# Performance work log

Measured on AMD Instinct MI355X. Metric: run time of the kernel, lower is better.

Reference implementation:

```python
import jax, jax.numpy as jnp
import numpy as np

HIDDEN = 1024
HEADS = 16
HEAD = HIDDEN // HEADS
EXPAND = 4096
EPS = 1e-5


def layer_norm(x, g, b):
    mu = jnp.mean(x, axis=-1, keepdims=True)
    var = jnp.mean((x - mu) ** 2, axis=-1, keepdims=True)
    return (x - mu) * jax.lax.rsqrt(var + EPS) * g + b


def setup_inputs() -> dict:
    key = jax.random.key(0)
    ks = jax.random.split(key, 12)
    s = 0.02
    return {
        "x": jax.random.normal(ks[0], (4, 2048, HIDDEN), dtype=jnp.float32),
        "Wqkv": jax.random.normal(ks[1], (HIDDEN, 3 * HIDDEN), dtype=jnp.float32) * s,
        "bqkv": jnp.zeros((3 * HIDDEN,), jnp.float32),
        "Wproj": jax.random.normal(ks[2], (HIDDEN, HIDDEN), dtype=jnp.float32) * s,
        "bproj": jnp.zeros((HIDDEN,), jnp.float32),
        "W1": jax.random.normal(ks[3], (HIDDEN, EXPAND), dtype=jnp.float32) * s,
        "b1": jnp.zeros((EXPAND,), jnp.float32),
        "W2": jax.random.normal(ks[4], (EXPAND, HIDDEN), dtype=jnp.float32) * s,
        "b2": jnp.zeros((HIDDEN,), jnp.float32),
        "g1": jnp.ones((HIDDEN,), jnp.float32),
        "be1": jnp.zeros((HIDDEN,), jnp.float32),
        "g2": jnp.ones((HIDDEN,), jnp.float32),
        "be2": jnp.zeros((HIDDEN,), jnp.float32),
    }


def attention(x, Wqkv, bqkv, Wproj, bproj):
    B, L, _ = x.shape
    qkv = (x @ Wqkv + bqkv).reshape(B, L, 3, HEADS, HEAD)
    q, k, v = [qkv[:, :, i].transpose(0, 2, 1, 3) for i in range(3)]  # [B,H,L,D]
    attn = jnp.einsum("bnld,bnkd->bnlk", q, k) / np.sqrt(HEAD).astype(np.float32)
    attn = jax.nn.softmax(attn, axis=-1)
    o = jnp.einsum("bnlk,bnkd->bnld", attn, v)
    o = o.transpose(0, 2, 1, 3).reshape(B, L, HIDDEN)
    return o @ Wproj + bproj


def reference(x, Wqkv, bqkv, Wproj, bproj, W1, b1, W2, b2, g1, be1, g2, be2):
    # post-norm transformer block (pre_norm=False), dropout=0 (eval)
    h = layer_norm(x + attention(x, Wqkv, bqkv, Wproj, bproj), g1, be1)
    ff = jax.nn.gelu(h @ W1 + b1, approximate=False) @ W2 + b2
    return layer_norm(h + ff, g2, be2)
```

## Files before the change

kernel.cpp:

```cpp
#include <hip/hip_runtime.h>
#include <hip/hip_bf16.h>
#include <math.h>


typedef __bf16 bf16_t;
typedef __bf16 bf16x8 __attribute__((ext_vector_type(8)));
typedef __bf16 bf16x4 __attribute__((ext_vector_type(4)));
typedef float f32x4 __attribute__((ext_vector_type(4)));
typedef float f32x16 __attribute__((ext_vector_type(16)));

#define HID   1024
#define NHEAD 16
#define HD    64
#define EXPD  4096
#define LSEQ  2048
#define BATCH 4
#define MROWS (BATCH * LSEQ)

#if __has_builtin(__builtin_amdgcn_exp2f)
#define EXP2F __builtin_amdgcn_exp2f
#else
#define EXP2F exp2f
#endif

__device__ __forceinline__ void gld_lds16(const bf16_t* g, bf16_t* l) {
  __builtin_amdgcn_global_load_lds(
      (const __attribute__((address_space(1))) void*)g,
      (__attribute__((address_space(3))) void*)l, 16, 0, 0);
}

template <int N>
__device__ __forceinline__ void wait_vm() {
  if constexpr (N == 8)      asm volatile("s_waitcnt vmcnt(8)" ::: "memory");
  else if constexpr (N == 6) asm volatile("s_waitcnt vmcnt(6)" ::: "memory");
  else if constexpr (N == 4) asm volatile("s_waitcnt vmcnt(4)" ::: "memory");
  else if constexpr (N == 3) asm volatile("s_waitcnt vmcnt(3)" ::: "memory");
  else                       asm volatile("s_waitcnt vmcnt(0)" ::: "memory");
}

__device__ __forceinline__ void swap32(unsigned& a, unsigned& b) {
#if __has_builtin(__builtin_amdgcn_permlane32_swap)
  auto r = __builtin_amdgcn_permlane32_swap(a, b, false, false);
  a = r[0]; b = r[1];
#else
  bool hiL = ((threadIdx.x & 63) >= 32);
  unsigned pa = (unsigned)__shfl_xor((int)a, 32, 64);
  unsigned pb = (unsigned)__shfl_xor((int)b, 32, 64);
  unsigned na = hiL ? pb : a;
  unsigned nb = hiL ? b : pa;
  a = na; b = nb;
#endif
}

__device__ __forceinline__ unsigned pk_bf16(float lo, float hi) {
  bf16_t l = (bf16_t)lo, h = (bf16_t)hi;
  unsigned short ul, uh;
  __builtin_memcpy(&ul, &l, 2);
  __builtin_memcpy(&uh, &h, 2);
  return (unsigned)ul | ((unsigned)uh << 16);
}

__global__ __launch_bounds__(256) void cvt_bf16(const float* __restrict__ in,
                                                bf16_t* __restrict__ out, int n4) {
  int i = blockIdx.x * 256 + threadIdx.x;
  if (i >= n4) return;
  float4 v = ((const float4*)in)[i];
  bf16x4 o;
  o[0] = (bf16_t)v.x; o[1] = (bf16_t)v.y; o[2] = (bf16_t)v.z; o[3] = (bf16_t)v.w;
  ((bf16x4*)out)[i] = o;
}

__global__ __launch_bounds__(256) void transpose_cvt(const float* __restrict__ W,
                                                     bf16_t* __restrict__ Wt,
                                                     int K, int N) {
  __shared__ float tile[32][33];
  int n0 = blockIdx.x * 32, k0 = blockIdx.y * 32;
  int tx = threadIdx.x & 31, ty = threadIdx.x >> 5;
#pragma unroll
  for (int i = 0; i < 32; i += 8)
    tile[ty + i][tx] = W[(size_t)(k0 + ty + i) * N + n0 + tx];
  __syncthreads();
#pragma unroll
  for (int i = 0; i < 32; i += 8)
    Wt[(size_t)(n0 + ty + i) * K + k0 + tx] = (bf16_t)tile[tx][ty + i];
}

__global__ __launch_bounds__(256) void transpose_v(const bf16_t* __restrict__ qkvb,
                                                   bf16_t* __restrict__ vT) {
  __shared__ bf16_t tile[64][65];
  const int l0 = blockIdx.x * 64;
  const int bh = blockIdx.y;
  const int b = bh >> 4, h = bh & 15;
  const int tx = threadIdx.x & 63, ty = threadIdx.x >> 6;
  const bf16_t* src = qkvb + ((size_t)(b * LSEQ + l0)) * 3072 + 2048 + h * 64;
#pragma unroll
  for (int i = 0; i < 16; ++i) {
    int l = ty + 4 * i;
    tile[l][tx] = src[(size_t)l * 3072 + tx];
  }
  __syncthreads();
  bf16_t* dst = vT + ((size_t)bh * HD) * LSEQ + l0;
#pragma unroll
  for (int i = 0; i < 16; ++i) {
    int d = ty + 4 * i;
    dst[(size_t)d * LSEQ + tx] = tile[tx][d];
  }
}

template <int BM>
__global__ __launch_bounds__(512, 2) void gemm_p(const bf16_t* __restrict__ A,
                                                 const bf16_t* __restrict__ Bt,
                                                 const float* __restrict__ bias,
                                                 void* __restrict__ C,
                                                 int M, int N, int K, int mode) {
  constexpr int MI = BM / 32;
  constexpr int LOADS = (BM == 256) ? 4 : 3;
  __shared__ bf16_t As[4 * BM * 32];
  __shared__ bf16_t Bs[4 * 256 * 32];

  const int nbx = gridDim.x;
  int p = blockIdx.y * nbx + blockIdx.x;
  const int GM = 8;
  int group = p / (GM * nbx);
  int idx = p - group * (GM * nbx);
  const int by = group * GM + (idx & (GM - 1));
  const int bx = idx >> 3;
  const int n0 = bx * 256, m0 = by * BM;

  const int t = threadIdx.x;
  const int lane = t & 63, w = t >> 6;
  const int wr = w >> 2, wc = w & 3;
  const int quad = lane >> 4, l16 = lane & 15;

  f32x4 acc[MI][4];
#pragma unroll
  for (int i = 0; i < MI; ++i)
#pragma unroll
    for (int j = 0; j < 4; ++j) acc[i][j] = (f32x4){0.f, 0.f, 0.f, 0.f};

  const int r0 = t >> 2;
  const unsigned ksw = (((unsigned)t & 3u) ^ ((unsigned)(r0 >> 1) & 3u)) * 8u;
  const unsigned offR0 = (unsigned)r0 * (unsigned)K + ksw;
  const unsigned off128 = offR0 + 128u * (unsigned)K;

  const bf16_t* aB = A + (size_t)m0 * K;
  const bf16_t* bB = Bt + (size_t)n0 * K;

  unsigned aoff[MI], boff[4];
#pragma unroll
  for (int i = 0; i < MI; ++i) {
    int row = wr * (BM / 2) + 16 * i + l16;
    aoff[i] = (unsigned)(row * 32 + (quad ^ ((row >> 1) & 3)) * 8);
  }
#pragma unroll
  for (int j = 0; j < 4; ++j) {
    int row = wc * 64 + 16 * j + l16;
    boff[j] = (unsigned)(row * 32 + (quad ^ ((row >> 1) & 3)) * 8);
  }

  auto stage = [&](int slot, int kk) {
    bf16_t* Asl = As + slot * (BM * 32);
    bf16_t* Bsl = Bs + slot * (256 * 32);
    const bf16_t* aS = aB + kk;
    const bf16_t* bS = bB + kk;
    gld_lds16(aS + offR0, Asl + t * 8);
    if constexpr (BM == 256) gld_lds16(aS + off128, Asl + (t + 512) * 8);
    gld_lds16(bS + offR0, Bsl + t * 8);
    gld_lds16(bS + off128, Bsl + (t + 512) * 8);
  };

  auto compute = [&](int slot) {
    const bf16_t* Asl = As + slot * (BM * 32);
    const bf16_t* Bsl = Bs + slot * (256 * 32);
    bf16x8 af[MI], bfr[4];
#pragma unroll
    for (int i = 0; i < MI; ++i) af[i] = *(const bf16x8*)(Asl + aoff[i]);
#pragma unroll
    for (int j = 0; j < 4; ++j) bfr[j] = *(const bf16x8*)(Bsl + boff[j]);
    __builtin_amdgcn_s_setprio(1);
#pragma unroll
    for (int i = 0; i < MI; ++i)
#pragma unroll
      for (int j = 0; j < 4; ++j)
        acc[i][j] = __builtin_amdgcn_mfma_f32_16x16x32_bf16(af[i], bfr[j], acc[i][j], 0, 0, 0);
    __builtin_amdgcn_s_setprio(0);
  };

  const int NT = K >> 5;

  stage(0, 0);
  stage(1, 32);
  stage(2, 64);
  int kk = 96;

  int kt = 0;
  for (; kt < NT - 3; ++kt) {
    wait_vm<2 * LOADS>();
    __builtin_amdgcn_s_barrier();
    asm volatile("" ::: "memory");
    stage((kt + 3) & 3, kk);
    kk += 32;
    compute(kt & 3);
  }
  wait_vm<2 * LOADS>();
  __builtin_amdgcn_s_barrier();
  asm volatile("" ::: "memory");
  compute(kt & 3);
  ++kt;
  wait_vm<LOADS>();
  __builtin_amdgcn_s_barrier();
  asm volatile("" ::: "memory");
  compute(kt & 3);
  ++kt;
  wait_vm<0>();
  __builtin_amdgcn_s_barrier();
  asm volatile("" ::: "memory");
  compute(kt & 3);

#pragma unroll
  for (int i = 0; i < MI; ++i) {
    int rowb = m0 + wr * (BM / 2) + 16 * i + quad * 4;
#pragma unroll
    for (int j = 0; j < 4; ++j) {
      int col = n0 + wc * 64 + 16 * j + l16;
      float bv = bias[col];
#pragma unroll
      for (int r = 0; r < 4; ++r) {
        float v = acc[i][j][r] + bv;
        size_t idx = (size_t)(rowb + r) * N + col;
        if (mode == 0) {
          ((bf16_t*)C)[idx] = (bf16_t)v;
        } else if (mode == 1) {
          float u = v * (0.7978845608028654f + 0.0356774081f * v * v);
          float e = EXP2F(u * 2.885390082f);
          float th = (e - 1.f) / (e + 1.f);
          float gel = 0.5f * v * (1.f + th);
          ((bf16_t*)C)[idx] = (bf16_t)gel;
        } else {
          ((float*)C)[idx] = v;
        }
      }
    }
  }
}

__global__ __launch_bounds__(256) void attn_kernel(const bf16_t* __restrict__ qkv,
                                                   const bf16_t* __restrict__ vT,
                                                   bf16_t* __restrict__ ob) {
  __shared__ bf16_t smem[3 * 128 * 64];
  bf16_t* Ks  = smem;
  bf16_t* Vts = smem + 8192;
  bf16_t* Qs  = smem + 16384;
  const int qt = blockIdx.x, h = blockIdx.y, b = blockIdx.z;
  const int t = threadIdx.x, lane = t & 63, w = t >> 6;
  const int l32 = lane & 31, hi = lane >> 5;
  const size_t RS = 3 * HID;
  const int bh = b * NHEAD + h;

  const bf16_t* qbase = qkv + ((size_t)(b * LSEQ + qt * 128)) * RS + h * HD;
  const bf16_t* kbase = qkv + ((size_t)b * LSEQ) * RS + HID + h * HD;
  const bf16_t* vtbase = vT + (size_t)bh * HD * LSEQ;

#pragma unroll
  for (int s = 0; s < 4; ++s) {
    int l = t + s * 256;
    int r = l >> 3, c8 = l & 7;
    gld_lds16(qbase + (size_t)r * RS + ((c8 ^ (r & 7)) * 8), Qs + l * 8);
  }
  __syncthreads();

  const float sc = 0.18033688011112042f;
  bf16x8 bq[4];
  {
    int qrow = 32 * w + l32;
#pragma unroll
    for (int c = 0; c < 4; ++c) {
      int y = 2 * c + hi;
      bf16x8 q8 = *(const bf16x8*)(Qs + qrow * 64 + ((y ^ (qrow & 7)) * 8));
#pragma unroll
      for (int e = 0; e < 8; ++e) q8[e] = (bf16_t)((float)q8[e] * sc);
      bq[c] = q8;
    }
  }

  f32x16 accO[2];
#pragma unroll
  for (int dt = 0; dt < 2; ++dt)
#pragma unroll
    for (int e = 0; e < 16; ++e) accO[dt][e] = 0.f;
  float l_acc = 0.f;

  for (int kt = 0; kt < LSEQ / 128; ++kt) {
    __syncthreads();
#pragma unroll
    for (int s = 0; s < 4; ++s) {
      int l = t + s * 256;
      int r = l >> 3, c8 = l & 7;
      gld_lds16(kbase + (size_t)(kt * 128 + r) * RS + ((c8 ^ (r & 7)) * 8), Ks + l * 8);
      int rv = l >> 4, c16 = l & 15;
      gld_lds16(vtbase + (size_t)rv * LSEQ + kt * 128 + ((c16 ^ (rv & 7)) * 8), Vts + l * 8);
    }
    __syncthreads();

#pragma unroll
    for (int kt2 = 0; kt2 < 2; ++kt2) {
      f32x16 s0, s1;
#pragma unroll
      for (int e = 0; e < 16; ++e) { s0[e] = 0.f; s1[e] = 0.f; }
#pragma unroll
      for (int c = 0; c < 4; ++c) {
        int y = 2 * c + hi;
        int r0 = (2 * kt2 + 0) * 32 + l32;
        bf16x8 a0 = *(const bf16x8*)(Ks + r0 * 64 + ((y ^ (r0 & 7)) * 8));
        s0 = __builtin_amdgcn_mfma_f32_32x32x16_bf16(a0, bq[c], s0, 0, 0, 0);
        int r1 = (2 * kt2 + 1) * 32 + l32;
        bf16x8 a1 = *(const bf16x8*)(Ks + r1 * 64 + ((y ^ (r1 & 7)) * 8));
        s1 = __builtin_amdgcn_mfma_f32_32x32x16_bf16(a1, bq[c], s1, 0, 0, 0);
      }

      unsigned pf[2][2][4];
#pragma unroll
      for (int tile = 0; tile < 2; ++tile) {
        f32x16& sv = tile ? s1 : s0;
        float p[16];
#pragma unroll
        for (int e = 0; e < 16; ++e) { p[e] = EXP2F(sv[e]); l_acc += p[e]; }
        unsigned lo[4], hi_[4];
#pragma unroll
        for (int g = 0; g < 4; ++g) {
          lo[g] = pk_bf16(p[4 * g + 0], p[4 * g + 1]);
          hi_[g] = pk_bf16(p[4 * g + 2], p[4 * g + 3]);
        }
#pragma unroll
        for (int c2 = 0; c2 < 2; ++c2) {
          unsigned aL = lo[2 * c2], bL = lo[2 * c2 + 1];
          swap32(aL, bL);
          pf[tile][c2][0] = aL; pf[tile][c2][2] = bL;
          unsigned aH = hi_[2 * c2], bH = hi_[2 * c2 + 1];
          swap32(aH, bH);
          pf[tile][c2][1] = aH; pf[tile][c2][3] = bH;
        }
      }

#pragma unroll
      for (int dt = 0; dt < 2; ++dt)
#pragma unroll
        for (int tile = 0; tile < 2; ++tile)
#pragma unroll
          for (int c2 = 0; c2 < 2; ++c2) {
            int ktile = 2 * kt2 + tile;
            int c8v = ktile * 4 + c2 * 2 + hi;
            int rv = dt * 32 + l32;
            bf16x8 av = *(const bf16x8*)(Vts + rv * 128 + ((c8v ^ (rv & 7)) * 8));
            union { unsigned u[4]; bf16x8 v; } bp;
            bp.u[0] = pf[tile][c2][0]; bp.u[1] = pf[tile][c2][1];
            bp.u[2] = pf[tile][c2][2]; bp.u[3] = pf[tile][c2][3];
            accO[dt] = __builtin_amdgcn_mfma_f32_32x32x16_bf16(av, bp.v, accO[dt], 0, 0, 0);
          }
    }
  }

  l_acc += __shfl_xor(l_acc, 32, 64);
  float inv = 1.f / l_acc;

  __syncthreads();
  bf16_t* Osh = smem;
  {
    int q = 32 * w + l32;
#pragma unroll
    for (int dt = 0; dt < 2; ++dt)
#pragma unroll
      for (int e = 0; e < 16; ++e) {
        int d = dt * 32 + (e & 3) + 8 * (e >> 2) + 4 * hi;
        Osh[q * 68 + d] = (bf16_t)(accO[dt][e] * inv);
      }
  }
  __syncthreads();
#pragma unroll
  for (int s = 0; s < 4; ++s) {
    int l = t + s * 256;
    int r = l >> 3, c8 = l & 7;
    bf16x8 v = *(const bf16x8*)(Osh + r * 68 + c8 * 8);
    *(bf16x8*)(ob + ((size_t)(b * LSEQ + qt * 128 + r)) * HID + h * HD + c8 * 8) = v;
  }
}

__global__ __launch_bounds__(256) void resid_ln(const float* __restrict__ X,
                                                const float* __restrict__ Y,
                                                const float* __restrict__ g,
                                                const float* __restrict__ be,
                                                float* __restrict__ outf,
                                                bf16_t* __restrict__ outb) {
  const int row = blockIdx.x;
  const int t = threadIdx.x;
  float4 a = ((const float4*)X)[(size_t)row * 256 + t];
  float4 bvec = ((const float4*)Y)[(size_t)row * 256 + t];
  float v0 = a.x + bvec.x, v1 = a.y + bvec.y, v2 = a.z + bvec.z, v3 = a.w + bvec.w;
  float s = v0 + v1 + v2 + v3;
  float s2 = v0 * v0 + v1 * v1 + v2 * v2 + v3 * v3;
#pragma unroll
  for (int msk = 1; msk < 64; msk <<= 1) {
    s += __shfl_xor(s, msk, 64);
    s2 += __shfl_xor(s2, msk, 64);
  }
  __shared__ float red[8];
  int w = t >> 6;
  if ((t & 63) == 0) { red[w] = s; red[w + 4] = s2; }
  __syncthreads();
  s = red[0] + red[1] + red[2] + red[3];
  s2 = red[4] + red[5] + red[6] + red[7];
  float mu = s * (1.f / 1024.f);
  float var = s2 * (1.f / 1024.f) - mu * mu;
  float rstd = rsqrtf(var + 1e-5f);
  float4 gg = ((const float4*)g)[t];
  float4 bb = ((const float4*)be)[t];
  float o0 = (v0 - mu) * rstd * gg.x + bb.x;
  float o1 = (v1 - mu) * rstd * gg.y + bb.y;
  float o2 = (v2 - mu) * rstd * gg.z + bb.z;
  float o3 = (v3 - mu) * rstd * gg.w + bb.w;
  float4 o = {o0, o1, o2, o3};
  ((float4*)outf)[(size_t)row * 256 + t] = o;
  if (outb) {
    bf16x4 ob4;
    ob4[0] = (bf16_t)o0; ob4[1] = (bf16_t)o1; ob4[2] = (bf16_t)o2; ob4[3] = (bf16_t)o3;
    ((bf16x4*)outb)[(size_t)row * 256 + t] = ob4;
  }
}

extern "C" void kernel_launch(void* const* d_in, const int* in_sizes, int n_in,
                              void* d_out, int out_size, void* d_ws, size_t ws_size,
                              hipStream_t stream) {
  const float* x     = (const float*)d_in[0];
  const float* Wqkv  = (const float*)d_in[1];
  const float* bqkv  = (const float*)d_in[2];
  const float* Wproj = (const float*)d_in[3];
  const float* bproj = (const float*)d_in[4];
  const float* W1    = (const float*)d_in[5];
  const float* b1    = (const float*)d_in[6];
  const float* W2    = (const float*)d_in[7];
  const float* b2    = (const float*)d_in[8];
  const float* g1    = (const float*)d_in[9];
  const float* be1   = (const float*)d_in[10];
  const float* g2    = (const float*)d_in[11];
  const float* be2   = (const float*)d_in[12];
  float* out = (float*)d_out;

  char* ws = (char*)d_ws;
  size_t off = 0;
  auto alloc = [&](size_t bytes) -> char* {
    char* p = ws + off;
    off += (bytes + 255) & ~(size_t)255;
    return p;
  };
  bf16_t* wqkvT  = (bf16_t*)alloc((size_t)3072 * 1024 * 2);
  bf16_t* wprojT = (bf16_t*)alloc((size_t)1024 * 1024 * 2);
  bf16_t* w1T    = (bf16_t*)alloc((size_t)4096 * 1024 * 2);
  bf16_t* w2T    = (bf16_t*)alloc((size_t)1024 * 4096 * 2);
  char*   xb_ob  = alloc((size_t)MROWS * HID * 2);
  char*   qkv_ff = alloc((size_t)MROWS * EXPD * 2);
  char*   a_f2   = alloc((size_t)MROWS * HID * 4);
  float*  h      = (float*)alloc((size_t)MROWS * HID * 4);
  bf16_t* hb     = (bf16_t*)alloc((size_t)MROWS * HID * 2);

  bf16_t* xb    = (bf16_t*)xb_ob;
  bf16_t* ob    = (bf16_t*)xb_ob;
  bf16_t* qkvb  = (bf16_t*)qkv_ff;
  bf16_t* ff1b  = (bf16_t*)qkv_ff;
  float*  attnf = (float*)a_f2;
  float*  ff2f  = (float*)a_f2;
  bf16_t* vTg   = hb;

  dim3 blk(256);
  dim3 blk512(512);
  transpose_cvt<<<dim3(3072 / 32, 1024 / 32), blk, 0, stream>>>(Wqkv, wqkvT, 1024, 3072);
  transpose_cvt<<<dim3(1024 / 32, 1024 / 32), blk, 0, stream>>>(Wproj, wprojT, 1024, 1024);
  transpose_cvt<<<dim3(4096 / 32, 1024 / 32), blk, 0, stream>>>(W1, w1T, 1024, 4096);
  transpose_cvt<<<dim3(1024 / 32, 4096 / 32), blk, 0, stream>>>(W2, w2T, 4096, 1024);
  cvt_bf16<<<MROWS * HID / 4 / 256, blk, 0, stream>>>(x, xb, MROWS * HID / 4);

  gemm_p<256><<<dim3(3072 / 256, MROWS / 256), blk512, 0, stream>>>(xb, wqkvT, bqkv, qkvb,
                                                                    MROWS, 3072, 1024, 0);
  transpose_v<<<dim3(LSEQ / 64, BATCH * NHEAD), blk, 0, stream>>>(qkvb, vTg);
  attn_kernel<<<dim3(LSEQ / 128, NHEAD, BATCH), blk, 0, stream>>>(qkvb, vTg, ob);
  gemm_p<128><<<dim3(1024 / 256, MROWS / 128), blk512, 0, stream>>>(ob, wprojT, bproj, attnf,
                                                                    MROWS, 1024, 1024, 2);
  resid_ln<<<MROWS, blk, 0, stream>>>(x, attnf, g1, be1, h, hb);
  gemm_p<256><<<dim3(4096 / 256, MROWS / 256), blk512, 0, stream>>>(hb, w1T, b1, ff1b,
                                                                    MROWS, 4096, 1024, 1);
  gemm_p<128><<<dim3(1024 / 256, MROWS / 128), blk512, 0, stream>>>(ff1b, w2T, b2, ff2f,
                                                                    MROWS, 1024, 4096, 2);
  resid_ln<<<MROWS, blk, 0, stream>>>(h, ff2f, g2, be2, out, (bf16_t*)nullptr);
}
```

Baseline: 630.5 us.

## Restructure GEMM k-step into two barrier-separated phases interleaving loads and MFMA

Replaces the GEMM main loop with a ping-pong style k-step: each iteration splits the MFMA work into two halves of the A rows. A and B global-to-LDS prefetches are interleaved between the halves, with explicit barriers, lgkmcnt waits and sched_barriers. The kernel is also re-parameterized on BN with BM fixed at 256, so the N=1024 GEMMs use 256x128 tiles instead of 128x256. The aim is better overlap of memory traffic with matrix math, at the cost of extra barriers per k-step and more fragile synchronization.

```diff
diff --git a/kernel.cpp b/kernel.cpp
--- a/kernel.cpp
+++ b/kernel.cpp
@@ -29,13 +29,12 @@
       (__attribute__((address_space(3))) void*)l, 16, 0, 0);
 }
 
-template <int N>
-__device__ __forceinline__ void wait_vm() {
-  if constexpr (N == 8)      asm volatile("s_waitcnt vmcnt(8)" ::: "memory");
-  else if constexpr (N == 6) asm volatile("s_waitcnt vmcnt(6)" ::: "memory");
-  else if constexpr (N == 4) asm volatile("s_waitcnt vmcnt(4)" ::: "memory");
-  else if constexpr (N == 3) asm volatile("s_waitcnt vmcnt(3)" ::: "memory");
-  else                       asm volatile("s_waitcnt vmcnt(0)" ::: "memory");
+__device__ __forceinline__ void vmwait(int n) {
+  if (n == 8)      asm volatile("s_waitcnt vmcnt(8)" ::: "memory");
+  else if (n == 6) asm volatile("s_waitcnt vmcnt(6)" ::: "memory");
+  else if (n == 4) asm volatile("s_waitcnt vmcnt(4)" ::: "memory");
+  else if (n == 3) asm volatile("s_waitcnt vmcnt(3)" ::: "memory");
+  else if (n == 0) asm volatile("s_waitcnt vmcnt(0)" ::: "memory");
 }
 
 __device__ __forceinline__ void swap32(unsigned& a, unsigned& b) {
@@ -107,16 +106,19 @@
   }
 }
 
-template <int BM>
-__global__ __launch_bounds__(512, 2) void gemm_p(const bf16_t* __restrict__ A,
-                                                 const bf16_t* __restrict__ Bt,
-                                                 const float* __restrict__ bias,
-                                                 void* __restrict__ C,
-                                                 int M, int N, int K, int mode) {
+template <int BN>
+__global__ __launch_bounds__(512, 2) void gemm_8p(const bf16_t* __restrict__ A,
+                                                  const bf16_t* __restrict__ Bt,
+                                                  const float* __restrict__ bias,
+                                                  void* __restrict__ C,
+                                                  int M, int N, int K, int mode) {
+  constexpr int BM = 256;
   constexpr int MI = BM / 32;
-  constexpr int LOADS = (BM == 256) ? 4 : 3;
+  constexpr int NJ = BN / 64;
+  constexpr int BL = BN / 128;
+  constexpr int LOADS = 2 + BL;
   __shared__ bf16_t As[4 * BM * 32];
-  __shared__ bf16_t Bs[4 * 256 * 32];
+  __shared__ bf16_t Bs[4 * BN * 32];
 
   const int nbx = gridDim.x;
   int p = blockIdx.y * nbx + blockIdx.x;
@@ -125,18 +127,18 @@
   int idx = p - group * (GM * nbx);
   const int by = group * GM + (idx & (GM - 1));
   const int bx = idx >> 3;
-  const int n0 = bx * 256, m0 = by * BM;
+  const int n0 = bx * BN, m0 = by * BM;
 
   const int t = threadIdx.x;
   const int lane = t & 63, w = t >> 6;
   const int wr = w >> 2, wc = w & 3;
   const int quad = lane >> 4, l16 = lane & 15;
 
-  f32x4 acc[MI][4];
+  f32x4 acc[MI][NJ];
 #pragma unroll
   for (int i = 0; i < MI; ++i)
 #pragma unroll
-    for (int j = 0; j < 4; ++j) acc[i][j] = (f32x4){0.f, 0.f, 0.f, 0.f};
+    for (int j = 0; j < NJ; ++j) acc[i][j] = (f32x4){0.f, 0.f, 0.f, 0.f};
 
   const int r0 = t >> 2;
   const unsigned ksw = (((unsigned)t & 3u) ^ ((unsigned)(r0 >> 1) & 3u)) * 8u;
@@ -146,83 +148,95 @@
   const bf16_t* aB = A + (size_t)m0 * K;
   const bf16_t* bB = Bt + (size_t)n0 * K;
 
-  unsigned aoff[MI], boff[4];
+  unsigned aoff[MI], boff[NJ];
 #pragma unroll
   for (int i = 0; i < MI; ++i) {
     int row = wr * (BM / 2) + 16 * i + l16;
     aoff[i] = (unsigned)(row * 32 + (quad ^ ((row >> 1) & 3)) * 8);
   }
 #pragma unroll
-  for (int j = 0; j < 4; ++j) {
-    int row = wc * 64 + 16 * j + l16;
+  for (int j = 0; j < NJ; ++j) {
+    int row = wc * (BN / 4) + 16 * j + l16;
     boff[j] = (unsigned)(row * 32 + (quad ^ ((row >> 1) & 3)) * 8);
   }
 
-  auto stage = [&](int slot, int kk) {
+  auto stageA = [&](int slot, int kk) {
     bf16_t* Asl = As + slot * (BM * 32);
-    bf16_t* Bsl = Bs + slot * (256 * 32);
     const bf16_t* aS = aB + kk;
+    gld_lds16(aS + offR0, Asl + t * 8);
+    gld_lds16(aS + off128, Asl + (t + 512) * 8);
+  };
+  auto stageB = [&](int slot, int kk) {
+    bf16_t* Bsl = Bs + slot * (BN * 32);
     const bf16_t* bS = bB + kk;
-    gld_lds16(aS + offR0, Asl + t * 8);
-    if constexpr (BM == 256) gld_lds16(aS + off128, Asl + (t + 512) * 8);
     gld_lds16(bS + offR0, Bsl + t * 8);
-    gld_lds16(bS + off128, Bsl + (t + 512) * 8);
+    if constexpr (BL == 2) gld_lds16(bS + off128, Bsl + (t + 512) * 8);
   };
 
-  auto compute = [&](int slot) {
+  auto kstep = [&](int slot, bool doStage, int kk, int waitN) {
     const bf16_t* Asl = As + slot * (BM * 32);
-    const bf16_t* Bsl = Bs + slot * (256 * 32);
-    bf16x8 af[MI], bfr[4];
-#pragma unroll
-    for (int i = 0; i < MI; ++i) af[i] = *(const bf16x8*)(Asl + aoff[i]);
-#pragma unroll
-    for (int j = 0; j < 4; ++j) bfr[j] = *(const bf16x8*)(Bsl + boff[j]);
+    const bf16_t* Bsl = Bs + slot * (BN * 32);
+    const int sslot = (slot + 3) & 3;
+    bf16x8 bfr[NJ], af[MI / 2];
+#pragma unroll
+    for (int i = 0; i < MI / 2; ++i) af[i] = *(const bf16x8*)(Asl + aoff[i]);
+#pragma unroll
+    for (int j = 0; j < NJ; ++j) bfr[j] = *(const bf16x8*)(Bsl + boff[j]);
+    if (doStage) stageA(sslot, kk);
+    __builtin_amdgcn_sched_barrier(0);
+    __builtin_amdgcn_s_barrier();
+    asm volatile("s_waitcnt lgkmcnt(0)" ::: "memory");
+    __builtin_amdgcn_sched_barrier(0);
     __builtin_amdgcn_s_setprio(1);
 #pragma unroll
-    for (int i = 0; i < MI; ++i)
-#pragma unroll
-      for (int j = 0; j < 4; ++j)
+    for (int i = 0; i < MI / 2; ++i)
+#pragma unroll
+      for (int j = 0; j < NJ; ++j)
         acc[i][j] = __builtin_amdgcn_mfma_f32_16x16x32_bf16(af[i], bfr[j], acc[i][j], 0, 0, 0);
     __builtin_amdgcn_s_setprio(0);
+    __builtin_amdgcn_sched_barrier(0);
+    __builtin_amdgcn_s_barrier();
+#pragma unroll
+    for (int i = 0; i < MI / 2; ++i) af[i] = *(const bf16x8*)(Asl + aoff[MI / 2 + i]);
+    if (doStage) stageB(sslot, kk);
+    vmwait(waitN);
+    __builtin_amdgcn_sched_barrier(0);
+    __builtin_amdgcn_s_barrier();
+    asm volatile("s_waitcnt lgkmcnt(0)" ::: "memory");
+    __builtin_amdgcn_sched_barrier(0);
+    __builtin_amdgcn_s_setprio(1);
+#pragma unroll
+    for (int i = 0; i < MI / 2; ++i)
+#pragma unroll
+      for (int j = 0; j < NJ; ++j)
+        acc[MI / 2 + i][j] =
+            __builtin_amdgcn_mfma_f32_16x16x32_bf16(af[i], bfr[j], acc[MI / 2 + i][j], 0, 0, 0);
+    __builtin_amdgcn_s_setprio(0);
+    __builtin_amdgcn_sched_barrier(0);
+    __builtin_amdgcn_s_barrier();
   };
 
   const int NT = K >> 5;
 
-  stage(0, 0);
-  stage(1, 32);
-  stage(2, 64);
-  int kk = 96;
+  stageA(0, 0);  stageB(0, 0);
+  stageA(1, 32); stageB(1, 32);
+  stageA(2, 64); stageB(2, 64);
+  vmwait(2 * LOADS);
+  __builtin_amdgcn_s_barrier();
 
   int kt = 0;
-  for (; kt < NT - 3; ++kt) {
-    wait_vm<2 * LOADS>();
-    __builtin_amdgcn_s_barrier();
-    asm volatile("" ::: "memory");
-    stage((kt + 3) & 3, kk);
-    kk += 32;
-    compute(kt & 3);
-  }
-  wait_vm<2 * LOADS>();
-  __builtin_amdgcn_s_barrier();
-  asm volatile("" ::: "memory");
-  compute(kt & 3);
-  ++kt;
-  wait_vm<LOADS>();
-  __builtin_amdgcn_s_barrier();
-  asm volatile("" ::: "memory");
-  compute(kt & 3);
-  ++kt;
-  wait_vm<0>();
-  __builtin_amdgcn_s_barrier();
-  asm volatile("" ::: "memory");
-  compute(kt & 3);
+  for (; kt < NT - 3; ++kt)
+    kstep(kt & 3, true, (kt + 3) * 32, 2 * LOADS);
+  kstep(kt & 3, false, 0, LOADS); ++kt;
+  kstep(kt & 3, false, 0, 0);     ++kt;
+  kstep(kt & 3, false, 0, -1);
 
 #pragma unroll
   for (int i = 0; i < MI; ++i) {
     int rowb = m0 + wr * (BM / 2) + 16 * i + quad * 4;
 #pragma unroll
-    for (int j = 0; j < 4; ++j) {
-      int col = n0 + wc * 64 + 16 * j + l16;
+    for (int j = 0; j < NJ; ++j) {
+      int col = n0 + wc * (BN / 4) + 16 * j + l16;
       float bv = bias[col];
 #pragma unroll
       for (int r = 0; r < 4; ++r) {
@@ -478,16 +492,16 @@
   transpose_cvt<<<dim3(1024 / 32, 4096 / 32), blk, 0, stream>>>(W2, w2T, 4096, 1024);
   cvt_bf16<<<MROWS * HID / 4 / 256, blk, 0, stream>>>(x, xb, MROWS * HID / 4);
 
-  gemm_p<256><<<dim3(3072 / 256, MROWS / 256), blk512, 0, stream>>>(xb, wqkvT, bqkv, qkvb,
-                                                                    MROWS, 3072, 1024, 0);
+  gemm_8p<256><<<dim3(3072 / 256, MROWS / 256), blk512, 0, stream>>>(xb, wqkvT, bqkv, qkvb,
+                                                                     MROWS, 3072, 1024, 0);
   transpose_v<<<dim3(LSEQ / 64, BATCH * NHEAD), blk, 0, stream>>>(qkvb, vTg);
   attn_kernel<<<dim3(LSEQ / 128, NHEAD, BATCH), blk, 0, stream>>>(qkvb, vTg, ob);
-  gemm_p<128><<<dim3(1024 / 256, MROWS / 128), blk512, 0, stream>>>(ob, wprojT, bproj, attnf,
-                                                                    MROWS, 1024, 1024, 2);
+  gemm_8p<128><<<dim3(1024 / 128, MROWS / 256), blk512, 0, stream>>>(ob, wprojT, bproj, attnf,
+                                                                     MROWS, 1024, 1024, 2);
   resid_ln<<<MROWS, blk, 0, stream>>>(x, attnf, g1, be1, h, hb);
-  gemm_p<256><<<dim3(4096 / 256, MROWS / 256), blk512, 0, stream>>>(hb, w1T, b1, ff1b,
-                                                                    MROWS, 4096, 1024, 1);
-  gemm_p<128><<<dim3(1024 / 256, MROWS / 128), blk512, 0, stream>>>(ff1b, w2T, b2, ff2f,
-                                                                    MROWS, 1024, 4096, 2);
+  gemm_8p<256><<<dim3(4096 / 256, MROWS / 256), blk512, 0, stream>>>(hb, w1T, b1, ff1b,
+                                                                     MROWS, 4096, 1024, 1);
+  gemm_8p<128><<<dim3(1024 / 128, MROWS / 256), blk512, 0, stream>>>(ff1b, w2T, b2, ff2f,
+                                                                     MROWS, 1024, 4096, 2);
   resid_ln<<<MROWS, blk, 0, stream>>>(h, ff2f, g2, be2, out, (bf16_t*)nullptr);
 }
```

Result: no change. 626.5 us (-0.6%).
